# Optimization experiments

Measured on AMD Instinct MI355X. Metric: run time of the kernel, lower is better.

## Reference

```python
import jax, jax.numpy as jnp
import numpy as np

N = 262144
E = N * 4  # kNN graph with K=4
D = 64

def setup_inputs() -> dict:
    key = jax.random.key(0)
    ks = jax.random.split(key, 16)
    s = 1.0 / np.sqrt(D)
    inp = {
        "x": jax.random.normal(ks[0], (N, D), jnp.float32),
        "edge_index": jax.random.randint(ks[1], (2, E), 0, N, dtype=jnp.int32).astype(jnp.int64),
        "sage_Wl": jax.random.normal(ks[2], (4, D, D), jnp.float32) * s,
        "sage_Wr": jax.random.normal(ks[3], (4, D, D), jnp.float32) * s,
        "sage_b": jnp.zeros((4, D), jnp.float32),
        "gat_W": jax.random.normal(ks[4], (3, D, D), jnp.float32) * s,
        "gat_a_src": jax.random.normal(ks[5], (3, D), jnp.float32) * s,
        "gat_a_dst": jax.random.normal(ks[6], (3, D), jnp.float32) * s,
        "gat_b": jnp.zeros((3, D), jnp.float32),
        "p1_W": jax.random.normal(ks[7], (64, 64), jnp.float32) * s,
        "p1_b": jnp.zeros((64,), jnp.float32),
        "p2_W": jax.random.normal(ks[8], (32, 64), jnp.float32) * s,
        "p2_b": jnp.zeros((32,), jnp.float32),
        "p3_W": jax.random.normal(ks[9], (16, 32), jnp.float32) * (1.0 / np.sqrt(32)),
        "p3_b": jnp.zeros((16,), jnp.float32),
    }
    return inp

def _sage_conv(x, src, dst, Wl, Wr, b, n):
    # mean-aggregate neighbor messages, then lin_l(agg) + lin_r(root)
    msg = x[src]                                               # [E, D]
    ssum = jax.ops.segment_sum(msg, dst, num_segments=n)       # [N, D]
    cnt = jax.ops.segment_sum(jnp.ones((src.shape[0], 1), x.dtype), dst, num_segments=n)
    mean = ssum / jnp.maximum(cnt, 1.0)
    return mean @ Wl.T + x @ Wr.T + b

def _gat_conv(x, src, dst, W, a_src, a_dst, b, n):
    # single-head GATConv with self-loops (PyG defaults)
    h = x @ W.T                                                # [N, D]
    asv = h @ a_src                                            # [N]
    adv = h @ a_dst                                            # [N]
    e = jax.nn.leaky_relu(asv[src] + adv[dst], 0.2)            # [E']
    m = jax.ops.segment_max(e, dst, num_segments=n)
    ee = jnp.exp(e - m[dst])
    denom = jax.ops.segment_sum(ee, dst, num_segments=n)
    alpha = ee / jnp.maximum(denom[dst], 1e-16)
    out = jax.ops.segment_sum(alpha[:, None] * h[src], dst, num_segments=n)
    return out + b

def reference(x, edge_index, sage_Wl, sage_Wr, sage_b,
              gat_W, gat_a_src, gat_a_dst, gat_b,
              p1_W, p1_b, p2_W, p2_b, p3_W, p3_b):
    n = x.shape[0]
    src, dst = edge_index[0], edge_index[1]
    # GraphSAGE: 4 layers, ReLU between layers (not after last)
    h = x
    for i in range(4):
        h = _sage_conv(h, src, dst, sage_Wl[i], sage_Wr[i], sage_b[i], n)
        if i < 3:
            h = jax.nn.relu(h)
    # GAT: 3 layers with self-loops, ReLU between layers
    loop = jnp.arange(n, dtype=src.dtype)
    src_sl = jnp.concatenate([src, loop])
    dst_sl = jnp.concatenate([dst, loop])
    for i in range(3):
        h = _gat_conv(h, src_sl, dst_sl, gat_W[i], gat_a_src[i], gat_a_dst[i], gat_b[i], n)
        if i < 2:
            h = jax.nn.relu(h)
    # ProjectionBlock (dropout inactive at inference)
    h = jax.nn.relu(h @ p1_W.T + p1_b)
    h = jax.nn.relu(h @ p2_W.T + p2_b)
    h = h @ p3_W.T + p3_b
    return h
```

## Files before the change

### kernel.cpp

```cpp
#include <hip/hip_runtime.h>
#include <type_traits>
#include <utility>

typedef __attribute__((ext_vector_type(4))) float f32x4;
typedef __attribute__((ext_vector_type(8))) short short8v;
typedef __attribute__((ext_vector_type(8))) unsigned short ushort8v;
typedef __attribute__((ext_vector_type(8))) __bf16 bf16x8;

template<typename T, typename = void> struct can_mfma : std::false_type {};
template<typename T> struct can_mfma<T, std::void_t<decltype(
  __builtin_amdgcn_mfma_f32_16x16x32_bf16(std::declval<T>(), std::declval<T>(),
                                          std::declval<f32x4>(), 0, 0, 0))>>
  : std::true_type {};
using frag_t = std::conditional_t<can_mfma<short8v>::value, short8v, bf16x8>;

__device__ __forceinline__ f32x4 MFMA(frag_t a, frag_t b, f32x4 c){
  return __builtin_amdgcn_mfma_f32_16x16x32_bf16(a, b, c, 0, 0, 0);
}

__device__ __forceinline__ unsigned short bfrn(float x){
  unsigned u = __float_as_uint(x);
  return (unsigned short)((u + 0x7FFFu + ((u >> 16) & 1u)) >> 16);
}
__device__ __forceinline__ float bf2f(unsigned short h){
  return __uint_as_float(((unsigned)h) << 16);
}
__device__ __forceinline__ float lrelu(float v){ return v > 0.f ? v : 0.2f*v; }
__device__ __forceinline__ void add4(float4& a, const float4 v){
  a.x += v.x; a.y += v.y; a.z += v.z; a.w += v.w; }
__device__ __forceinline__ void fma4(float4& a, float w, const float4 v){
  a.x += w*v.x; a.y += w*v.y; a.z += w*v.z; a.w += w*v.w; }
__device__ __forceinline__ void mul4(float4& a, float w){
  a.x *= w; a.y *= w; a.z *= w; a.w *= w; }

__device__ __forceinline__ void split8(const float* vals, frag_t& fh, frag_t& fl){
  union { unsigned short u[8]; ushort8v v; } Uh, Ul;
#pragma unroll
  for (int j = 0; j < 8; j++){
    unsigned short hb = bfrn(vals[j]);
    Uh.u[j] = hb;
    Ul.u[j] = bfrn(vals[j] - bf2f(hb));
  }
  fh = __builtin_bit_cast(frag_t, Uh.v);
  fl = __builtin_bit_cast(frag_t, Ul.v);
}

__global__ void deg_count(const int* __restrict__ dst, int* __restrict__ deg, int E){
  int e = blockIdx.x*blockDim.x + threadIdx.x;
  if (e < E) atomicAdd(&deg[dst[e]], 1);
}

__global__ void scan_block(const int* __restrict__ deg, int* __restrict__ rowptr,
                           int* __restrict__ bsum){
  __shared__ int s[256];
  int t = threadIdx.x; int i = blockIdx.x*256 + t;
  int v = deg[i];
  s[t] = v; __syncthreads();
  for (int off=1; off<256; off<<=1){
    int a = (t>=off)? s[t-off] : 0; __syncthreads();
    s[t] += a; __syncthreads();
  }
  rowptr[i+1] = s[t];
  if (t==255) bsum[blockIdx.x] = s[255];
}

__global__ void scan_top(int* __restrict__ bsum){
  __shared__ int s[256];
  int t = threadIdx.x;
  int v0=bsum[t*4], v1=bsum[t*4+1], v2=bsum[t*4+2], v3=bsum[t*4+3];
  s[t] = v0+v1+v2+v3; __syncthreads();
  for (int off=1; off<256; off<<=1){
    int a = (t>=off)? s[t-off] : 0; __syncthreads();
    s[t] += a; __syncthreads();
  }
  int excl = (t==0)? 0 : s[t-1];
  bsum[t*4]   = excl;
  bsum[t*4+1] = excl+v0;
  bsum[t*4+2] = excl+v0+v1;
  bsum[t*4+3] = excl+v0+v1+v2;
}

__global__ void scan_add_wp(int* __restrict__ rowptr, int* __restrict__ wp,
                            const int* __restrict__ bsum){
  int i = blockIdx.x*256 + threadIdx.x;
  int v = rowptr[i+1] + bsum[blockIdx.x];
  rowptr[i+1] = v;
  wp[i+1] = v;
  if (i == 0){ rowptr[0] = 0; wp[0] = 0; }
}

__global__ void fill_csr(const int* __restrict__ src, const int* __restrict__ dst,
                         int* __restrict__ wp, int* __restrict__ col, int E){
  int e = blockIdx.x*blockDim.x + threadIdx.x;
  if (e < E){
    int d = dst[e];
    int pos = atomicAdd(&wp[d], 1);
    __builtin_nontemporal_store(src[e], &col[pos]);
  }
}

__global__ void prep_weights(const float* __restrict__ Wl, const float* __restrict__ Wr,
                             const float* __restrict__ Wg, const float* __restrict__ P1,
                             const float* __restrict__ P2, const float* __restrict__ P3,
                             unsigned short* __restrict__ hi, unsigned short* __restrict__ lo){
  int i = blockIdx.x*256 + threadIdx.x;
  if (i >= 51712) return;
  float v;
  if (i < 16384) v = Wl[i];
  else if (i < 32768) v = Wr[i-16384];
  else if (i < 45056) v = Wg[i-32768];
  else if (i < 49152) v = P1[i-45056];
  else if (i < 51200) v = P2[i-49152];
  else v = P3[i-51200];
  unsigned short hb = bfrn(v);
  hi[i] = hb;
  lo[i] = bfrn(v - bf2f(hb));
}

__global__ __launch_bounds__(256,3) void sage_mfma(
    const float* __restrict__ cur, const int* __restrict__ rowptr,
    const int* __restrict__ col,
    const unsigned short* __restrict__ WlHi, const unsigned short* __restrict__ WlLo,
    const unsigned short* __restrict__ WrHi, const unsigned short* __restrict__ WrLo,
    const float* __restrict__ bias, float* __restrict__ out, int do_relu){
  __shared__ __align__(16) unsigned short sMhi[64*64];
  __shared__ __align__(16) unsigned short sMlo[64*64];
  __shared__ __align__(16) unsigned short sW[4][4096];
  int t = threadIdx.x;
  int row0 = blockIdx.x * 64;
  int w = t >> 6, l = t & 63;
  int lr = l & 15, lg = l >> 4;
  {
    const ushort8v* g0 = (const ushort8v*)WlHi;
    const ushort8v* g1 = (const ushort8v*)WlLo;
    const ushort8v* g2 = (const ushort8v*)WrHi;
    const ushort8v* g3 = (const ushort8v*)WrLo;
#pragma unroll
    for (int i = 0; i < 2; i++){
      int c = t + i*256;
      int row = c >> 3, slot = c & 7;
      int addr = row*64 + ((slot ^ (row & 7)) << 3);
      *(ushort8v*)&sW[0][addr] = g0[c];
      *(ushort8v*)&sW[1][addr] = g1[c];
      *(ushort8v*)&sW[2][addr] = g2[c];
      *(ushort8v*)&sW[3][addr] = g3[c];
    }
  }
  {
    int o = l & 7;
    int rw = l >> 3;
    const float4* base4 = (const float4*)cur;
#pragma unroll
    for (int p = 0; p < 2; p++){
      int r = p*32 + w*8 + rw;
      int row = row0 + r;
      int beg = rowptr[row], end = rowptr[row+1];
      float4 a0 = {0,0,0,0}, a1 = a0;
      for (int j = beg; j < end; j += 4){
        int e1i = end - 1;
        int i1 = j+1 < end ? j+1 : e1i;
        int i2 = j+2 < end ? j+2 : e1i;
        int i3 = j+3 < end ? j+3 : e1i;
        int s0 = col[j], s1 = col[i1], s2 = col[i2], s3 = col[i3];
        float w1 = (j+1<end)?1.f:0.f, w2=(j+2<end)?1.f:0.f, w3=(j+3<end)?1.f:0.f;
        const float4* p0 = base4 + (size_t)s0*16 + o*2;
        const float4* p1 = base4 + (size_t)s1*16 + o*2;
        const float4* p2 = base4 + (size_t)s2*16 + o*2;
        const float4* p3 = base4 + (size_t)s3*16 + o*2;
        float4 q00=p0[0], q01=p0[1], q10=p1[0], q11=p1[1];
        float4 q20=p2[0], q21=p2[1], q30=p3[0], q31=p3[1];
        add4(a0,q00);    add4(a1,q01);
        fma4(a0,w1,q10); fma4(a1,w1,q11);
        fma4(a0,w2,q20); fma4(a1,w2,q21);
        fma4(a0,w3,q30); fma4(a1,w3,q31);
      }
      float rdeg = 1.f / fmaxf((float)(end-beg), 1.f);
      mul4(a0,rdeg); mul4(a1,rdeg);
      float mv[8];
      *(float4*)&mv[0] = a0; *(float4*)&mv[4] = a1;
      union { unsigned short u[8]; ushort8v v; } Uh, Ul;
#pragma unroll
      for (int j2 = 0; j2 < 8; j2++){
        unsigned short hb = bfrn(mv[j2]);
        Uh.u[j2] = hb;
        Ul.u[j2] = bfrn(mv[j2] - bf2f(hb));
      }
      int slot = o ^ (r & 7);
      *(ushort8v*)&sMhi[r*64 + slot*8] = Uh.v;
      *(ushort8v*)&sMlo[r*64 + slot*8] = Ul.v;
    }
  }
  frag_t ax_hi[2], ax_lo[2];
  {
    int grow = row0 + w*16 + lr;
#pragma unroll
    for (int kt = 0; kt < 2; kt++){
      float vals[8];
      const float* p = cur + (size_t)grow*64 + kt*32 + lg*8;
      *(float4*)&vals[0] = *(const float4*)p;
      *(float4*)&vals[4] = *(const float4*)(p + 4);
      split8(vals, ax_hi[kt], ax_lo[kt]);
    }
  }
  __syncthreads();
  int rl = (w << 4) + lr;
  frag_t am_hi[2], am_lo[2];
#pragma unroll
  for (int kt = 0; kt < 2; kt++){
    int slot = (kt*4 + lg) ^ (rl & 7);
    am_hi[kt] = __builtin_bit_cast(frag_t, *(const ushort8v*)&sMhi[rl*64 + slot*8]);
    am_lo[kt] = __builtin_bit_cast(frag_t, *(const ushort8v*)&sMlo[rl*64 + slot*8]);
  }
#pragma unroll
  for (int ct = 0; ct < 4; ct++){
    float bv = bias[ct*16 + lr];
    f32x4 acc = {bv, bv, bv, bv};
    int wrow = ct*16 + lr;
#pragma unroll
    for (int kt = 0; kt < 2; kt++){
      int sl = wrow*64 + (((kt*4 + lg) ^ (wrow & 7)) << 3);
      frag_t blh = __builtin_bit_cast(frag_t, *(const ushort8v*)&sW[0][sl]);
      frag_t bll = __builtin_bit_cast(frag_t, *(const ushort8v*)&sW[1][sl]);
      acc = MFMA(am_hi[kt], blh, acc);
      acc = MFMA(am_lo[kt], blh, acc);
      acc = MFMA(am_hi[kt], bll, acc);
      frag_t brh = __builtin_bit_cast(frag_t, *(const ushort8v*)&sW[2][sl]);
      frag_t brl = __builtin_bit_cast(frag_t, *(const ushort8v*)&sW[3][sl]);
      acc = MFMA(ax_hi[kt], brh, acc);
      acc = MFMA(ax_lo[kt], brh, acc);
      acc = MFMA(ax_hi[kt], brl, acc);
    }
#pragma unroll
    for (int r = 0; r < 4; r++){
      float v = acc[r];
      if (do_relu) v = fmaxf(v, 0.f);
      out[(size_t)(row0 + w*16 + lg*4 + r)*64 + ct*16 + lr] = v;
    }
  }
}

__global__ __launch_bounds__(256,8) void gat_mfma(
    const float* __restrict__ cur,
    const unsigned short* __restrict__ WHi, const unsigned short* __restrict__ WLo,
    const float* __restrict__ a_src, const float* __restrict__ a_dst,
    float* __restrict__ h, float* __restrict__ asv, float* __restrict__ adv){
  __shared__ __align__(16) unsigned short sW[2][4096];
  int t = threadIdx.x;
  int row0 = blockIdx.x * 64;
  int w = t >> 6, l = t & 63;
  int lr = l & 15, lg = l >> 4;
  {
    const ushort8v* g0 = (const ushort8v*)WHi;
    const ushort8v* g1 = (const ushort8v*)WLo;
#pragma unroll
    for (int i = 0; i < 2; i++){
      int c = t + i*256;
      int row = c >> 3, slot = c & 7;
      int addr = row*64 + ((slot ^ (row & 7)) << 3);
      *(ushort8v*)&sW[0][addr] = g0[c];
      *(ushort8v*)&sW[1][addr] = g1[c];
    }
  }
  frag_t ax_hi[2], ax_lo[2];
  {
    int grow = row0 + w*16 + lr;
#pragma unroll
    for (int kt = 0; kt < 2; kt++){
      float vals[8];
      const float* p = cur + (size_t)grow*64 + kt*32 + lg*8;
      *(float4*)&vals[0] = *(const float4*)p;
      *(float4*)&vals[4] = *(const float4*)(p + 4);
      split8(vals, ax_hi[kt], ax_lo[kt]);
    }
  }
  __syncthreads();
  float pav[4] = {0,0,0,0}, pdv[4] = {0,0,0,0};
#pragma unroll
  for (int ct = 0; ct < 4; ct++){
    f32x4 acc = {0,0,0,0};
    int wrow = ct*16 + lr;
#pragma unroll
    for (int kt = 0; kt < 2; kt++){
      int sl = wrow*64 + (((kt*4 + lg) ^ (wrow & 7)) << 3);
      frag_t bh = __builtin_bit_cast(frag_t, *(const ushort8v*)&sW[0][sl]);
      frag_t bl = __builtin_bit_cast(frag_t, *(const ushort8v*)&sW[1][sl]);
      acc = MFMA(ax_hi[kt], bh, acc);
      acc = MFMA(ax_lo[kt], bh, acc);
      acc = MFMA(ax_hi[kt], bl, acc);
    }
    float asc = a_src[ct*16 + lr], adc = a_dst[ct*16 + lr];
#pragma unroll
    for (int r = 0; r < 4; r++){
      float v = acc[r];
      h[(size_t)(row0 + w*16 + lg*4 + r)*64 + ct*16 + lr] = v;
      pav[r] += v * asc;
      pdv[r] += v * adc;
    }
  }
#pragma unroll
  for (int off = 1; off < 16; off <<= 1){
#pragma unroll
    for (int r = 0; r < 4; r++){
      pav[r] += __shfl_xor(pav[r], off);
      pdv[r] += __shfl_xor(pdv[r], off);
    }
  }
  if (lr == 0){
#pragma unroll
    for (int r = 0; r < 4; r++){
      int row = row0 + w*16 + lg*4 + r;
      asv[row] = pav[r];
      adv[row] = pdv[r];
    }
  }
}

__global__ __launch_bounds__(256,6) void gat_agg(
    const float* __restrict__ h, const int* __restrict__ rowptr,
    const int* __restrict__ col, const float* __restrict__ asv,
    const float* __restrict__ adv, const float* __restrict__ bias,
    float* __restrict__ out, int do_relu){
  int t = threadIdx.x;
  int row0 = blockIdx.x * 32;
  int rl = t >> 3;
  int o = t & 7;
  int v = row0 + rl;
  int beg = rowptr[v], end = rowptr[v+1];
  float advv = adv[v];
  float m = lrelu(asv[v] + advv);
  float den = 1.f;
  const float4* hb4 = (const float4*)h;
  const float4* pv = hb4 + (size_t)v*16 + o*2;
  float4 a0 = pv[0], a1 = pv[1];
  for (int j = beg; j < end; j += 4){
    int e1i = end - 1;
    int i1 = j+1 < end ? j+1 : e1i;
    int i2 = j+2 < end ? j+2 : e1i;
    int i3 = j+3 < end ? j+3 : e1i;
    int s0 = col[j], s1 = col[i1], s2 = col[i2], s3 = col[i3];
    float q1 = (j+1<end)?1.f:0.f, q2=(j+2<end)?1.f:0.f, q3=(j+3<end)?1.f:0.f;
    float e0 = lrelu(asv[s0] + advv);
    float e1 = lrelu(asv[s1] + advv);
    float e2 = lrelu(asv[s2] + advv);
    float e3 = lrelu(asv[s3] + advv);
    float cm = fmaxf(fmaxf(e0, e1), fmaxf(e2, e3));
    if (cm > m){
      float sc = expf(m - cm);
      den *= sc; mul4(a0, sc); mul4(a1, sc);
      m = cm;
    }
    float w0 = expf(e0 - m);
    float w1 = q1 * expf(e1 - m);
    float w2 = q2 * expf(e2 - m);
    float w3 = q3 * expf(e3 - m);
    den += w0 + w1 + w2 + w3;
    const float4* p0 = hb4 + (size_t)s0*16 + o*2;
    const float4* p1 = hb4 + (size_t)s1*16 + o*2;
    const float4* p2 = hb4 + (size_t)s2*16 + o*2;
    const float4* p3 = hb4 + (size_t)s3*16 + o*2;
    float4 g00=p0[0], g01=p0[1], g10=p1[0], g11=p1[1];
    float4 g20=p2[0], g21=p2[1], g30=p3[0], g31=p3[1];
    fma4(a0,w0,g00); fma4(a1,w0,g01);
    fma4(a0,w1,g10); fma4(a1,w1,g11);
    fma4(a0,w2,g20); fma4(a1,w2,g21);
    fma4(a0,w3,g30); fma4(a1,w3,g31);
  }
  float rden = 1.f / fmaxf(den, 1e-16f);
  const float4* b4 = (const float4*)bias;
  float4 bb0 = b4[o*2], bb1 = b4[o*2+1];
  mul4(a0,rden); mul4(a1,rden);
  add4(a0,bb0); add4(a1,bb1);
  if (do_relu){
    a0.x=fmaxf(a0.x,0.f); a0.y=fmaxf(a0.y,0.f); a0.z=fmaxf(a0.z,0.f); a0.w=fmaxf(a0.w,0.f);
    a1.x=fmaxf(a1.x,0.f); a1.y=fmaxf(a1.y,0.f); a1.z=fmaxf(a1.z,0.f); a1.w=fmaxf(a1.w,0.f);
  }
  float4* o4 = (float4*)out + (size_t)v*16 + o*2;
  o4[0] = a0; o4[1] = a1;
}

__global__ __launch_bounds__(256,3) void mlp3(
    const float* __restrict__ in,
    const unsigned short* __restrict__ W1Hi, const unsigned short* __restrict__ W1Lo,
    const unsigned short* __restrict__ W2Hi, const unsigned short* __restrict__ W2Lo,
    const unsigned short* __restrict__ W3Hi, const unsigned short* __restrict__ W3Lo,
    const float* __restrict__ b1, const float* __restrict__ b2,
    const float* __restrict__ b3, float* __restrict__ out){
  __shared__ __align__(16) unsigned short sW1[2][4096];
  __shared__ __align__(16) unsigned short sW2[2][2048];
  __shared__ __align__(16) unsigned short sW3[2][512];
  __shared__ float sH1[64*68];
  __shared__ float sH2[64*36];
  int t = threadIdx.x;
  int row0 = blockIdx.x * 64;
  int w = t >> 6, l = t & 63;
  int lr = l & 15, lg = l >> 4;
  {
#pragma unroll
    for (int i = 0; i < 2; i++){
      int c = t + i*256;
      int row = c >> 3, slot = c & 7;
      int addr = row*64 + ((slot ^ (row & 7)) << 3);
      *(ushort8v*)&sW1[0][addr] = ((const ushort8v*)W1Hi)[c];
      *(ushort8v*)&sW1[1][addr] = ((const ushort8v*)W1Lo)[c];
    }
    {
      int c = t;
      int row = c >> 3, slot = c & 7;
      int addr = row*64 + ((slot ^ (row & 7)) << 3);
      *(ushort8v*)&sW2[0][addr] = ((const ushort8v*)W2Hi)[c];
      *(ushort8v*)&sW2[1][addr] = ((const ushort8v*)W2Lo)[c];
    }
    if (t < 64){
      int row = t >> 2, slot = t & 3;
      int addr = row*32 + ((slot ^ (row & 3)) << 3);
      *(ushort8v*)&sW3[0][addr] = ((const ushort8v*)W3Hi)[t];
      *(ushort8v*)&sW3[1][addr] = ((const ushort8v*)W3Lo)[t];
    }
  }
  frag_t ax_hi[2], ax_lo[2];
  {
    int grow = row0 + w*16 + lr;
#pragma unroll
    for (int kt = 0; kt < 2; kt++){
      float vals[8];
      const float* p = in + (size_t)grow*64 + kt*32 + lg*8;
      *(float4*)&vals[0] = *(const float4*)p;
      *(float4*)&vals[4] = *(const float4*)(p + 4);
      split8(vals, ax_hi[kt], ax_lo[kt]);
    }
  }
  __syncthreads();
#pragma unroll
  for (int ct = 0; ct < 4; ct++){
    int wrow = ct*16 + lr;
    float bv = b1[wrow];
    f32x4 acc = {bv, bv, bv, bv};
#pragma unroll
    for (int kt = 0; kt < 2; kt++){
      int sl = wrow*64 + (((kt*4 + lg) ^ (wrow & 7)) << 3);
      frag_t bh = __builtin_bit_cast(frag_t, *(const ushort8v*)&sW1[0][sl]);
      frag_t bl = __builtin_bit_cast(frag_t, *(const ushort8v*)&sW1[1][sl]);
      acc = MFMA(ax_hi[kt], bh, acc);
      acc = MFMA(ax_lo[kt], bh, acc);
      acc = MFMA(ax_hi[kt], bl, acc);
    }
#pragma unroll
    for (int r = 0; r < 4; r++)
      sH1[(w*16 + lg*4 + r)*68 + wrow] = fmaxf(acc[r], 0.f);
  }
  frag_t a2_hi[2], a2_lo[2];
#pragma unroll
  for (int kt = 0; kt < 2; kt++){
    float vals[8];
    const float* p = &sH1[(w*16 + lr)*68 + kt*32 + lg*8];
    *(float4*)&vals[0] = *(const float4*)p;
    *(float4*)&vals[4] = *(const float4*)(p + 4);
    split8(vals, a2_hi[kt], a2_lo[kt]);
  }
#pragma unroll
  for (int ct = 0; ct < 2; ct++){
    int wrow = ct*16 + lr;
    float bv = b2[wrow];
    f32x4 acc = {bv, bv, bv, bv};
#pragma unroll
    for (int kt = 0; kt < 2; kt++){
      int sl = wrow*64 + (((kt*4 + lg) ^ (wrow & 7)) << 3);
      frag_t bh = __builtin_bit_cast(frag_t, *(const ushort8v*)&sW2[0][sl]);
      frag_t bl = __builtin_bit_cast(frag_t, *(const ushort8v*)&sW2[1][sl]);
      acc = MFMA(a2_hi[kt], bh, acc);
      acc = MFMA(a2_lo[kt], bh, acc);
      acc = MFMA(a2_hi[kt], bl, acc);
    }
#pragma unroll
    for (int r = 0; r < 4; r++)
      sH2[(w*16 + lg*4 + r)*36 + wrow] = fmaxf(acc[r], 0.f);
  }
  frag_t a3_hi, a3_lo;
  {
    float vals[8];
    const float* p = &sH2[(w*16 + lr)*36 + lg*8];
    *(float4*)&vals[0] = *(const float4*)p;
    *(float4*)&vals[4] = *(const float4*)(p + 4);
    split8(vals, a3_hi, a3_lo);
  }
  {
    float bv = b3[lr];
    f32x4 acc = {bv, bv, bv, bv};
    int sl = lr*32 + ((lg ^ (lr & 3)) << 3);
    frag_t bh = __builtin_bit_cast(frag_t, *(const ushort8v*)&sW3[0][sl]);
    frag_t bl = __builtin_bit_cast(frag_t, *(const ushort8v*)&sW3[1][sl]);
    acc = MFMA(a3_hi, bh, acc);
    acc = MFMA(a3_lo, bh, acc);
    acc = MFMA(a3_hi, bl, acc);
#pragma unroll
    for (int r = 0; r < 4; r++)
      out[(size_t)(row0 + w*16 + lg*4 + r)*16 + lr] = acc[r];
  }
}

extern "C" void kernel_launch(void* const* d_in, const int* in_sizes, int n_in,
                              void* d_out, int out_size, void* d_ws, size_t ws_size,
                              hipStream_t stream) {
    const float* x        = (const float*)d_in[0];
    const int*   ei       = (const int*)d_in[1];
    const float* sage_Wl  = (const float*)d_in[2];
    const float* sage_Wr  = (const float*)d_in[3];
    const float* sage_b   = (const float*)d_in[4];
    const float* gat_W    = (const float*)d_in[5];
    const float* gat_as   = (const float*)d_in[6];
    const float* gat_ad   = (const float*)d_in[7];
    const float* gat_b    = (const float*)d_in[8];
    const float* p1W = (const float*)d_in[9],  *p1b = (const float*)d_in[10];
    const float* p2W = (const float*)d_in[11], *p2b = (const float*)d_in[12];
    const float* p3W = (const float*)d_in[13], *p3b = (const float*)d_in[14];

    int n = in_sizes[0] / 64;
    int E = in_sizes[1] / 2;
    const int* src = ei;
    const int* dst = ei + E;

    size_t N64 = (size_t)n * 64;
    float* bufA   = (float*)d_ws;
    float* bufB   = bufA + N64;
    int*   rowptr = (int*)(bufB + N64);
    int*   wp     = rowptr + (n + 4);
    int*   col    = wp + (n + 4);
    int*   bsum   = col + E;
    float* asv    = (float*)(bsum + 1024);
    float* adv    = asv + n;

    unsigned short* whi = (unsigned short*)(adv + n);
    unsigned short* wlo = whi + 51712;

    int nb = n / 256;

    hipMemsetAsync(wp, 0, (size_t)n * 4, stream);
    deg_count<<<(E + 255) / 256, 256, 0, stream>>>(dst, wp, E);
    scan_block<<<nb, 256, 0, stream>>>(wp, rowptr, bsum);
    scan_top<<<1, 256, 0, stream>>>(bsum);
    scan_add_wp<<<nb, 256, 0, stream>>>(rowptr, wp, bsum);
    fill_csr<<<(E + 255) / 256, 256, 0, stream>>>(src, dst, wp, col, E);

    prep_weights<<<202, 256, 0, stream>>>(sage_Wl, sage_Wr, gat_W, p1W, p2W, p3W,
                                          whi, wlo);

    const float* cur = x;
    float* nxt = bufA;
    for (int l = 0; l < 4; l++){
        sage_mfma<<<n / 64, 256, 0, stream>>>(cur, rowptr, col,
            whi + l*4096,          wlo + l*4096,
            whi + 16384 + l*4096,  wlo + 16384 + l*4096,
            sage_b + l*64, nxt, l < 3 ? 1 : 0);
        cur = nxt;
        nxt = (nxt == bufA) ? bufB : bufA;
    }

    for (int l = 0; l < 3; l++){
        gat_mfma<<<n / 64, 256, 0, stream>>>(cur,
            whi + 32768 + l*4096, wlo + 32768 + l*4096,
            gat_as + l*64, gat_ad + l*64, nxt, asv, adv);
        gat_agg<<<n / 32, 256, 0, stream>>>(nxt, rowptr, col, asv, adv,
            gat_b + l*64, (float*)cur, l < 2 ? 1 : 0);
    }

    mlp3<<<n / 64, 256, 0, stream>>>(cur,
        whi + 45056, wlo + 45056,
        whi + 49152, wlo + 49152,
        whi + 51200, wlo + 51200,
        p1b, p2b, p3b, (float*)d_out);
}
```

Before: 668.5 us.

## Build CSR via two-level bucket sort with shared-memory atomics

Replaces the global-atomic degree count, three-kernel scan and global-atomic CSR fill with a bucketed counting sort. Edges are first grouped into 256 coarse buckets of 1024 destinations using block-local histograms, then each bucket is sorted locally in shared memory to produce rowptr and col. This avoids heavy contended global atomics and scattered writes, at the cost of an extra packed record buffer and a hardcoded assumption that n is 256*1024 and source ids fit in 18 bits.

```diff
diff --git a/kernel.cpp b/kernel.cpp
--- a/kernel.cpp
+++ b/kernel.cpp
@@ -45,57 +45,100 @@
   fl = __builtin_bit_cast(frag_t, Ul.v);
 }
 
-__global__ void deg_count(const int* __restrict__ dst, int* __restrict__ deg, int E){
-  int e = blockIdx.x*blockDim.x + threadIdx.x;
-  if (e < E) atomicAdd(&deg[dst[e]], 1);
-}
-
-__global__ void scan_block(const int* __restrict__ deg, int* __restrict__ rowptr,
-                           int* __restrict__ bsum){
+
+__global__ void bucket_hist(const int* __restrict__ dst, int* __restrict__ bcnt, int E){
+  __shared__ int h[256];
+  int t = threadIdx.x;
+  h[t] = 0; __syncthreads();
+  int base = blockIdx.x * 4096;
+#pragma unroll
+  for (int i = 0; i < 16; i++){
+    int e = base + t + i*256;
+    if (e < E) atomicAdd(&h[dst[e] >> 10], 1);
+  }
+  __syncthreads();
+  atomicAdd(&bcnt[t], h[t]);
+}
+
+__global__ void bucket_scan(const int* __restrict__ bcnt, int* __restrict__ boff,
+                            int* __restrict__ bcur){
   __shared__ int s[256];
-  int t = threadIdx.x; int i = blockIdx.x*256 + t;
-  int v = deg[i];
+  int t = threadIdx.x;
+  int v = bcnt[t];
   s[t] = v; __syncthreads();
   for (int off=1; off<256; off<<=1){
     int a = (t>=off)? s[t-off] : 0; __syncthreads();
     s[t] += a; __syncthreads();
   }
-  rowptr[i+1] = s[t];
-  if (t==255) bsum[blockIdx.x] = s[255];
-}
-
-__global__ void scan_top(int* __restrict__ bsum){
-  __shared__ int s[256];
-  int t = threadIdx.x;
-  int v0=bsum[t*4], v1=bsum[t*4+1], v2=bsum[t*4+2], v3=bsum[t*4+3];
-  s[t] = v0+v1+v2+v3; __syncthreads();
+  boff[t+1] = s[t];
+  bcur[t] = s[t] - v;
+  if (t == 0) boff[0] = 0;
+}
+
+__global__ void bucket_scatter(const int* __restrict__ src, const int* __restrict__ dst,
+                               int* __restrict__ bcur, unsigned* __restrict__ rec, int E){
+  __shared__ int h[256], hb[256];
+  int t = threadIdx.x;
+  h[t] = 0; __syncthreads();
+  int base = blockIdx.x * 4096;
+#pragma unroll
+  for (int i = 0; i < 16; i++){
+    int e = base + t + i*256;
+    if (e < E) atomicAdd(&h[dst[e] >> 10], 1);
+  }
+  __syncthreads();
+  hb[t] = atomicAdd(&bcur[t], h[t]);
+  h[t] = 0;
+  __syncthreads();
+#pragma unroll
+  for (int i = 0; i < 16; i++){
+    int e = base + t + i*256;
+    if (e < E){
+      int d = dst[e];
+      int b = d >> 10;
+      int lp = atomicAdd(&h[b], 1);
+      rec[hb[b] + lp] = (unsigned)src[e] | ((unsigned)(d & 1023) << 18);
+    }
+  }
+}
+
+__global__ __launch_bounds__(256) void bucket_fill(
+    const unsigned* __restrict__ rec, const int* __restrict__ boff,
+    int* __restrict__ rowptr, int* __restrict__ col){
+  __shared__ int cnt[1024];
+  __shared__ int stmp[256];
+  int t = threadIdx.x;
+  int b = blockIdx.x;
+  int base = boff[b];
+  int m = boff[b+1] - base;
+#pragma unroll
+  for (int i = 0; i < 4; i++) cnt[t*4+i] = 0;
+  __syncthreads();
+  for (int j = t; j < m; j += 256)
+    atomicAdd(&cnt[rec[base+j] >> 18], 1);
+  __syncthreads();
+  int c0=cnt[t*4], c1=cnt[t*4+1], c2=cnt[t*4+2], c3=cnt[t*4+3];
+  int s = c0+c1+c2+c3;
+  stmp[t] = s; __syncthreads();
   for (int off=1; off<256; off<<=1){
-    int a = (t>=off)? s[t-off] : 0; __syncthreads();
-    s[t] += a; __syncthreads();
-  }
-  int excl = (t==0)? 0 : s[t-1];
-  bsum[t*4]   = excl;
-  bsum[t*4+1] = excl+v0;
-  bsum[t*4+2] = excl+v0+v1;
-  bsum[t*4+3] = excl+v0+v1+v2;
-}
-
-__global__ void scan_add_wp(int* __restrict__ rowptr, int* __restrict__ wp,
-                            const int* __restrict__ bsum){
-  int i = blockIdx.x*256 + threadIdx.x;
-  int v = rowptr[i+1] + bsum[blockIdx.x];
-  rowptr[i+1] = v;
-  wp[i+1] = v;
-  if (i == 0){ rowptr[0] = 0; wp[0] = 0; }
-}
-
-__global__ void fill_csr(const int* __restrict__ src, const int* __restrict__ dst,
-                         int* __restrict__ wp, int* __restrict__ col, int E){
-  int e = blockIdx.x*blockDim.x + threadIdx.x;
-  if (e < E){
-    int d = dst[e];
-    int pos = atomicAdd(&wp[d], 1);
-    __builtin_nontemporal_store(src[e], &col[pos]);
+    int a = (t>=off)? stmp[t-off] : 0; __syncthreads();
+    stmp[t] += a; __syncthreads();
+  }
+  int excl = stmp[t] - s;
+  int e0 = excl, e1 = e0+c0, e2 = e1+c1, e3 = e2+c2;
+  cnt[t*4]=e0; cnt[t*4+1]=e1; cnt[t*4+2]=e2; cnt[t*4+3]=e3;
+  int vbase = b*1024 + t*4;
+  rowptr[vbase+1] = base + e1;
+  rowptr[vbase+2] = base + e2;
+  rowptr[vbase+3] = base + e3;
+  rowptr[vbase+4] = base + e3 + c3;
+  if (b == 0 && t == 0) rowptr[0] = 0;
+  __syncthreads();
+  for (int j = t; j < m; j += 256){
+    unsigned r = rec[base+j];
+    int d = r >> 18;
+    int p = atomicAdd(&cnt[d], 1);
+    col[base + p] = (int)(r & 0x3FFFFu);
   }
 }
 
@@ -520,26 +563,27 @@
     const int* dst = ei + E;
 
     size_t N64 = (size_t)n * 64;
-    float* bufA   = (float*)d_ws;
-    float* bufB   = bufA + N64;
-    int*   rowptr = (int*)(bufB + N64);
-    int*   wp     = rowptr + (n + 4);
-    int*   col    = wp + (n + 4);
-    int*   bsum   = col + E;
-    float* asv    = (float*)(bsum + 1024);
-    float* adv    = asv + n;
-
+    float* bufA     = (float*)d_ws;
+    float* bufB     = bufA + N64;
+    int*   rowptr   = (int*)(bufB + N64);
+    int*   col      = rowptr + (n + 4);
+    unsigned* rec   = (unsigned*)(col + E);
+    int*   bcnt     = (int*)(rec + E);
+    int*   boff     = bcnt + 256;
+    int*   bcur     = boff + 260;
+    float* asv      = (float*)(bcur + 256);
+    float* adv      = asv + n;
     unsigned short* whi = (unsigned short*)(adv + n);
     unsigned short* wlo = whi + 51712;
 
-    int nb = n / 256;
-
-    hipMemsetAsync(wp, 0, (size_t)n * 4, stream);
-    deg_count<<<(E + 255) / 256, 256, 0, stream>>>(dst, wp, E);
-    scan_block<<<nb, 256, 0, stream>>>(wp, rowptr, bsum);
-    scan_top<<<1, 256, 0, stream>>>(bsum);
-    scan_add_wp<<<nb, 256, 0, stream>>>(rowptr, wp, bsum);
-    fill_csr<<<(E + 255) / 256, 256, 0, stream>>>(src, dst, wp, col, E);
+    int nbk = (E + 4095) / 4096;
+    int nbu = n / 1024;
+
+    hipMemsetAsync(bcnt, 0, 256 * 4, stream);
+    bucket_hist<<<nbk, 256, 0, stream>>>(dst, bcnt, E);
+    bucket_scan<<<1, 256, 0, stream>>>(bcnt, boff, bcur);
+    bucket_scatter<<<nbk, 256, 0, stream>>>(src, dst, bcur, rec, E);
+    bucket_fill<<<nbu, 256, 0, stream>>>(rec, boff, rowptr, col);
 
     prep_weights<<<202, 256, 0, stream>>>(sage_Wl, sage_Wr, gat_W, p1W, p2W, p3W,
                                           whi, wlo);
```

Result: faster. 586.5 us (-12.3%).
